# Performance work log

Measured on AMD Instinct MI355X. Metric: run time of the kernel, lower is better.

The kernel has to match this reference:

```python
import jax, jax.numpy as jnp
import numpy as np

N_NODES = 100000
N_EDGES = 300000
F_IN = 128
H = 256
L = 3


def setup_inputs() -> dict:
    key = jax.random.key(0)
    ks = jax.random.split(key, 8)
    s = 0.05
    return {
        "x": jax.random.normal(ks[0], (N_NODES, F_IN), dtype=jnp.float32),
        "edge_index": jax.random.randint(ks[1], (2, N_EDGES), 0, N_NODES, dtype=jnp.int32),
        "enc_w1": jax.random.normal(ks[2], (F_IN, H), dtype=jnp.float32) * s,
        "enc_b1": jnp.zeros((H,), dtype=jnp.float32),
        "enc_w2": jax.random.normal(ks[3], (H, H), dtype=jnp.float32) * s,
        "enc_b2": jnp.zeros((H,), dtype=jnp.float32),
        "gcn_w": jax.random.normal(ks[4], (L, H, H), dtype=jnp.float32) * s,
        "gcn_b": jnp.zeros((L, H), dtype=jnp.float32),
    }


def reference(x, edge_index, enc_w1, enc_b1, enc_w2, enc_b2, gcn_w, gcn_b):
    N = x.shape[0]
    # node_encoder: Linear -> ReLU -> (Dropout=id in eval) -> Linear
    h = jax.nn.relu(x @ enc_w1 + enc_b1) @ enc_w2 + enc_b2  # [N, H]

    # GCNConv normalization with self-loops (PyG default)
    loops = jnp.arange(N, dtype=edge_index.dtype)
    src = jnp.concatenate([edge_index[0], loops])  # [E+N]
    dst = jnp.concatenate([edge_index[1], loops])
    deg = jax.ops.segment_sum(jnp.ones_like(dst, dtype=h.dtype), dst, num_segments=N)
    dinv = jnp.where(deg > 0, jax.lax.rsqrt(deg), 0.0)
    norm = (dinv[src] * dinv[dst])[:, None]  # [E+N, 1]

    num_layers = gcn_w.shape[0]
    for l in range(num_layers):
        m = h @ gcn_w[l]  # transform [N, H]
        # gather messages from src, normalize, scatter-add to dst
        h = jax.ops.segment_sum(m[src] * norm, dst, num_segments=N) + gcn_b[l]
        h = jax.nn.relu(h)  # dropout is identity in eval mode
    return h
```

## Files before the change

### kernel.cpp

```cpp
#include <hip/hip_runtime.h>
#include <hip/hip_bf16.h>

#define NNODES 100000
#define NEDGES 300000
#define FIN 128
#define HDIM 256
#define NLAYERS 3
#define MPAD 100096

typedef float f32x4 __attribute__((ext_vector_type(4)));
typedef short bf16x8 __attribute__((ext_vector_type(8)));

__device__ inline float bf2f(unsigned short u) {
    union { unsigned int i; float f; } v;
    v.i = ((unsigned int)u) << 16;
    return v.f;
}
__device__ inline unsigned short f2bf(float f) {
    union { float f; unsigned int i; } v;
    v.f = f;
    return (unsigned short)((v.i + 0x7fffu + ((v.i >> 16) & 1u)) >> 16);
}

__device__ __forceinline__ void gll16(const unsigned short* g, unsigned short* l) {
    __builtin_amdgcn_global_load_lds(
        (const __attribute__((address_space(1))) unsigned int*)g,
        (__attribute__((address_space(3))) unsigned int*)l, 16, 0, 0);
}

template <int K, bool BIAS, bool RELU>
__global__ __launch_bounds__(256) void gemm_lds_k(
    const unsigned short* __restrict__ A, const unsigned short* __restrict__ Bt,
    const float* __restrict__ bias, unsigned short* __restrict__ C) {
    constexpr int BK = 32;
    constexpr int NT = K / BK;
    __shared__ unsigned short sA[3][128 * BK];
    __shared__ unsigned short sB[3][128 * BK];

    const int tid  = threadIdx.x;
    const int lane = tid & 63;
    const int wid  = tid >> 6;
    const int r15  = lane & 15;
    const int kq   = lane >> 4;
    const int wr   = wid >> 1;
    const int wc   = wid & 1;
    const int rowblk = blockIdx.y * 128;
    const int colblk = blockIdx.x * 128;

    const unsigned short* gA[2];
    const unsigned short* gB[2];
    int ldsbase[2];
#pragma unroll
    for (int q = 0; q < 2; ++q) {
        int rr   = q * 64 + wid * 16 + (lane >> 2);
        int slot = (lane & 3) ^ ((rr >> 1) & 3);
        gA[q] = A  + (size_t)(rowblk + rr) * K + slot * 8;
        gB[q] = Bt + (size_t)(colblk + rr) * K + slot * 8;
        ldsbase[q] = (q * 64 + wid * 16) * BK;
    }

    const int sread = ((kq ^ ((r15 >> 1) & 3)) * 8);
    int aoff[4], boff[4];
#pragma unroll
    for (int i = 0; i < 4; ++i) {
        aoff[i] = (wr * 64 + i * 16 + r15) * BK + sread;
        boff[i] = (wc * 64 + i * 16 + r15) * BK + sread;
    }

    f32x4 acc[4][4] = {};

#pragma unroll
    for (int q = 0; q < 2; ++q) {
        gll16(gA[q], &sA[0][ldsbase[q]]);
        gll16(gB[q], &sB[0][ldsbase[q]]);
    }
#pragma unroll
    for (int q = 0; q < 2; ++q) {
        gll16(gA[q] + BK, &sA[1][ldsbase[q]]);
        gll16(gB[q] + BK, &sB[1][ldsbase[q]]);
    }

#pragma unroll
    for (int t = 0; t < NT; ++t) {
        if (t + 1 < NT) {
            asm volatile("s_waitcnt vmcnt(4)" ::: "memory");
        } else {
            asm volatile("s_waitcnt vmcnt(0)" ::: "memory");
        }
        __builtin_amdgcn_s_barrier();
        if (t + 2 < NT) {
#pragma unroll
            for (int q = 0; q < 2; ++q) {
                gll16(gA[q] + (t + 2) * BK, &sA[(t + 2) % 3][ldsbase[q]]);
                gll16(gB[q] + (t + 2) * BK, &sB[(t + 2) % 3][ldsbase[q]]);
            }
        }
        bf16x8 a[4], b[4];
#pragma unroll
        for (int i = 0; i < 4; ++i) a[i] = *(const bf16x8*)&sA[t % 3][aoff[i]];
#pragma unroll
        for (int j = 0; j < 4; ++j) b[j] = *(const bf16x8*)&sB[t % 3][boff[j]];
#pragma unroll
        for (int i = 0; i < 4; ++i)
#pragma unroll
            for (int j = 0; j < 4; ++j)
                acc[i][j] = __builtin_amdgcn_mfma_f32_16x16x32_bf16(a[i], b[j], acc[i][j], 0, 0, 0);
    }

#pragma unroll
    for (int i = 0; i < 4; ++i) {
#pragma unroll
        for (int reg = 0; reg < 4; ++reg) {
            int row = rowblk + wr * 64 + i * 16 + kq * 4 + reg;
#pragma unroll
            for (int j = 0; j < 4; ++j) {
                int col = colblk + wc * 64 + j * 16 + r15;
                float v = acc[i][j][reg];
                if (BIAS) v += bias[col];
                if (RELU) v = fmaxf(v, 0.0f);
                C[(size_t)row * HDIM + col] = f2bf(v);
            }
        }
    }
}

__global__ void wprep_k(const float* __restrict__ W, unsigned short* __restrict__ Wt,
                        int K, int total) {
    int i = blockIdx.x * blockDim.x + threadIdx.x;
    if (i >= total) return;
    int mat = i / (K * 256);
    int r = i - mat * (K * 256);
    int k = r >> 8, p = r & 255;
    Wt[(size_t)mat * K * 256 + (size_t)p * K + k] = f2bf(W[i]);
}

__global__ void conv_k(const float* __restrict__ W, unsigned short* __restrict__ o, int n4) {
    int i = blockIdx.x * blockDim.x + threadIdx.x;
    if (i >= n4) return;
    float4 v = ((const float4*)W)[i];
    ushort4 u;
    u.x = f2bf(v.x); u.y = f2bf(v.y); u.z = f2bf(v.z); u.w = f2bf(v.w);
    ((ushort4*)o)[i] = u;
}

__global__ void foldbias_k(const float* __restrict__ b2, const float* __restrict__ g0,
                           float* __restrict__ fb) {
    int c = threadIdx.x;
    float s = 0.0f;
#pragma unroll 8
    for (int j = 0; j < HDIM; ++j) s += b2[j] * g0[(size_t)j * HDIM + c];
    fb[c] = s;
}

__global__ void zero_k(unsigned* __restrict__ p, int n) {
    int i = blockIdx.x * blockDim.x + threadIdx.x;
    if (i < n) p[i] = 0u;
}

__global__ void count_k(const int* __restrict__ dst, unsigned* __restrict__ cnt, int E) {
    int e = blockIdx.x * blockDim.x + threadIdx.x;
    if (e < E) atomicAdd(&cnt[dst[e]], 1u);
}

__global__ __launch_bounds__(256) void scan1_k(unsigned* __restrict__ cnt,
                                               int* __restrict__ rs,
                                               unsigned* __restrict__ blocksum,
                                               float* __restrict__ dinv, int N) {
    __shared__ unsigned tmp[256];
    int tid = threadIdx.x;
    int gid = blockIdx.x * 256 + tid;
    unsigned v = (gid < N) ? cnt[gid] : 0u;
    if (gid < N) {
        dinv[gid] = 1.0f / sqrtf((float)(v + 1u));
        cnt[gid] = 0u;
    }
    tmp[tid] = v;
    __syncthreads();
#pragma unroll
    for (int off = 1; off < 256; off <<= 1) {
        unsigned t = (tid >= off) ? tmp[tid - off] : 0u;
        __syncthreads();
        tmp[tid] += t;
        __syncthreads();
    }
    if (gid < N) rs[gid] = (int)(tmp[tid] - v);
    if (tid == 255) blocksum[blockIdx.x] = tmp[tid];
}

__global__ __launch_bounds__(512) void scan2_k(unsigned* __restrict__ blocksum, int nb) {
    __shared__ unsigned tmp[512];
    int tid = threadIdx.x;
    unsigned v = (tid < nb) ? blocksum[tid] : 0u;
    tmp[tid] = v;
    __syncthreads();
#pragma unroll
    for (int off = 1; off < 512; off <<= 1) {
        unsigned t = (tid >= off) ? tmp[tid - off] : 0u;
        __syncthreads();
        tmp[tid] += t;
        __syncthreads();
    }
    if (tid < nb) blocksum[tid] = tmp[tid] - v;
}

__global__ void scan3_k(int* __restrict__ rs, const unsigned* __restrict__ blocksum, int N, int E) {
    int gid = blockIdx.x * blockDim.x + threadIdx.x;
    if (gid < N) rs[gid] += (int)blocksum[gid >> 8];
    if (gid == 0) rs[N] = E;
}

__global__ void fill_k(const int* __restrict__ src, const int* __restrict__ dst,
                       const int* __restrict__ rs, unsigned* __restrict__ cursor,
                       const float* __restrict__ dinv,
                       int2* __restrict__ edata, int E) {
    int e = blockIdx.x * blockDim.x + threadIdx.x;
    if (e >= E) return;
    int s = src[e], d = dst[e];
    int pos = rs[d] + (int)atomicAdd(&cursor[d], 1u);
    float w = dinv[s] * dinv[d];
    edata[pos] = make_int2(s, __float_as_int(w));
}

template <bool OUTF32>
__global__ __launch_bounds__(256) void gather_k(const int* __restrict__ rs,
                                                const int2* __restrict__ edata,
                                                const float* __restrict__ dinv,
                                                const unsigned short* __restrict__ m,
                                                const float* __restrict__ bias,
                                                void* __restrict__ out, int N) {
    int node = blockIdx.x * 4 + (threadIdx.x >> 6);
    int lane = threadIdx.x & 63;
    if (node >= N) return;
    int beg = rs[node], end = rs[node + 1];
    float d = dinv[node];
    float w0 = d * d;
    ushort4 u = ((const ushort4*)(m + (size_t)node * HDIM))[lane];
    float ax = bf2f(u.x) * w0, ay = bf2f(u.y) * w0, az = bf2f(u.z) * w0, aw = bf2f(u.w) * w0;

    for (int base = beg; base < end; base += 64) {
        int2 ed = (base + lane < end) ? edata[base + lane] : make_int2(0, 0);
        int take = end - base;
        if (take > 64) take = 64;
        for (int e = 0; e < take; e += 4) {
            int s0 = __shfl(ed.x, e + 0);
            int s1 = __shfl(ed.x, e + 1);
            int s2 = __shfl(ed.x, e + 2);
            int s3 = __shfl(ed.x, e + 3);
            float wq0 = __int_as_float(__shfl(ed.y, e + 0));
            float wq1 = __int_as_float(__shfl(ed.y, e + 1));
            float wq2 = __int_as_float(__shfl(ed.y, e + 2));
            float wq3 = __int_as_float(__shfl(ed.y, e + 3));
            ushort4 v0 = ((const ushort4*)(m + (size_t)s0 * HDIM))[lane];
            ushort4 v1 = ((const ushort4*)(m + (size_t)s1 * HDIM))[lane];
            ushort4 v2 = ((const ushort4*)(m + (size_t)s2 * HDIM))[lane];
            ushort4 v3 = ((const ushort4*)(m + (size_t)s3 * HDIM))[lane];
            ax += bf2f(v0.x) * wq0; ay += bf2f(v0.y) * wq0;
            az += bf2f(v0.z) * wq0; aw += bf2f(v0.w) * wq0;
            ax += bf2f(v1.x) * wq1; ay += bf2f(v1.y) * wq1;
            az += bf2f(v1.z) * wq1; aw += bf2f(v1.w) * wq1;
            ax += bf2f(v2.x) * wq2; ay += bf2f(v2.y) * wq2;
            az += bf2f(v2.z) * wq2; aw += bf2f(v2.w) * wq2;
            ax += bf2f(v3.x) * wq3; ay += bf2f(v3.y) * wq3;
            az += bf2f(v3.z) * wq3; aw += bf2f(v3.w) * wq3;
        }
    }

    float4 b = ((const float4*)bias)[lane];
    ax = fmaxf(ax + b.x, 0.0f);
    ay = fmaxf(ay + b.y, 0.0f);
    az = fmaxf(az + b.z, 0.0f);
    aw = fmaxf(aw + b.w, 0.0f);
    if (OUTF32) {
        float4 o = {ax, ay, az, aw};
        ((float4*)out)[(size_t)node * 64 + lane] = o;
    } else {
        ushort4 o;
        o.x = f2bf(ax); o.y = f2bf(ay); o.z = f2bf(az); o.w = f2bf(aw);
        ((ushort4*)out)[(size_t)node * 64 + lane] = o;
    }
}

extern "C" void kernel_launch(void* const* d_in, const int* in_sizes, int n_in,
                              void* d_out, int out_size, void* d_ws, size_t ws_size,
                              hipStream_t stream) {
    const float* x  = (const float*)d_in[0];
    const int* ei   = (const int*)d_in[1];
    const float* w1 = (const float*)d_in[2];
    const float* b1 = (const float*)d_in[3];
    const float* w2 = (const float*)d_in[4];
    const float* b2 = (const float*)d_in[5];
    const float* gw = (const float*)d_in[6];
    const float* gb = (const float*)d_in[7];

    const int N = NNODES, E = NEDGES;
    const int* src = ei;
    const int* dst = ei + E;

    char* p = (char*)d_ws;
    unsigned short* h1   = (unsigned short*)p; p += (size_t)MPAD * HDIM * 2;
    unsigned short* h    = (unsigned short*)p; p += (size_t)MPAD * HDIM * 2;
    unsigned short* m    = (unsigned short*)p; p += (size_t)MPAD * HDIM * 2;
    unsigned short* w1t  = (unsigned short*)p; p += (size_t)FIN * HDIM * 2;
    unsigned short* gwt  = (unsigned short*)p; p += (size_t)NLAYERS * HDIM * HDIM * 2;
    unsigned short* w2c  = (unsigned short*)p; p += (size_t)HDIM * HDIM * 2;
    unsigned short* fBt  = (unsigned short*)p; p += (size_t)HDIM * HDIM * 2;
    float* foldb = (float*)p;          p += (size_t)HDIM * 4;
    unsigned* cnt = (unsigned*)p;      p += (size_t)N * 4;
    float* dinv = (float*)p;           p += (size_t)N * 4;
    int* rs = (int*)p;                 p += (size_t)(N + 1) * 4 + 12;
    unsigned* blocksum = (unsigned*)p; p += 512 * 4;
    int2* edata = (int2*)p;            p += (size_t)E * 8;

    unsigned short* xb = m;

    const int nb = (N + 255) / 256;
    const dim3 ggrid(2, MPAD / 128);

    wprep_k<<<(FIN * 256 + 255) / 256, 256, 0, stream>>>(w1, w1t, FIN, FIN * 256);
    wprep_k<<<(NLAYERS * HDIM * 256 + 255) / 256, 256, 0, stream>>>(gw, gwt, HDIM, NLAYERS * HDIM * 256);
    conv_k<<<(HDIM * HDIM / 4 + 255) / 256, 256, 0, stream>>>(w2, w2c, HDIM * HDIM / 4);
    conv_k<<<(N * FIN / 4 + 255) / 256, 256, 0, stream>>>(x, xb, N * FIN / 4);

    foldbias_k<<<1, 256, 0, stream>>>(b2, gw, foldb);
    gemm_lds_k<HDIM, false, false><<<dim3(2, 2), 256, 0, stream>>>(gwt, w2c, nullptr, fBt);

    zero_k<<<nb, 256, 0, stream>>>(cnt, N);
    count_k<<<(E + 255) / 256, 256, 0, stream>>>(dst, cnt, E);
    scan1_k<<<nb, 256, 0, stream>>>(cnt, rs, blocksum, dinv, N);
    scan2_k<<<1, 512, 0, stream>>>(blocksum, nb);
    scan3_k<<<nb + 1, 256, 0, stream>>>(rs, blocksum, N, E);
    fill_k<<<(E + 255) / 256, 256, 0, stream>>>(src, dst, rs, cnt, dinv, edata, E);

    gemm_lds_k<FIN, true, true><<<ggrid, 256, 0, stream>>>(xb, w1t, b1, h1);

    gemm_lds_k<HDIM, true, false><<<ggrid, 256, 0, stream>>>(h1, fBt, foldb, m);
    gather_k<false><<<(N + 3) / 4, 256, 0, stream>>>(rs, edata, dinv, m, gb, h, N);

    for (int l = 1; l < NLAYERS; ++l) {
        const unsigned short* wl = gwt + (size_t)l * HDIM * HDIM;
        const float* bl = gb + (size_t)l * HDIM;
        gemm_lds_k<HDIM, false, false><<<ggrid, 256, 0, stream>>>(h, wl, nullptr, m);
        if (l < NLAYERS - 1)
            gather_k<false><<<(N + 3) / 4, 256, 0, stream>>>(rs, edata, dinv, m, bl, h, N);
        else
            gather_k<true><<<(N + 3) / 4, 256, 0, stream>>>(rs, edata, dinv, m, bl, d_out, N);
    }
}
```

Before: 459.8 us.

## Widen GEMM tile to full 256 columns with 512-thread blocks and vectorized stores

The GEMM kernel now uses 8 waves per block covering a 128x256 output tile, so each block spans the full hidden width and the grid drops to one column block. Each A row tile is loaded once instead of twice across column blocks. The MFMA operands are swapped so each lane holds four consecutive columns, which allows packed 4-element bf16 stores and a float4 bias load. The trade-off is more LDS per block (B tile doubled) and fewer blocks in flight, which may lower occupancy.

```diff
diff --git a/kernel.cpp b/kernel.cpp
--- a/kernel.cpp
+++ b/kernel.cpp
@@ -29,34 +29,36 @@
 }
 
 template <int K, bool BIAS, bool RELU>
-__global__ __launch_bounds__(256) void gemm_lds_k(
+__global__ __launch_bounds__(512, 4) void gemm_lds_k(
     const unsigned short* __restrict__ A, const unsigned short* __restrict__ Bt,
     const float* __restrict__ bias, unsigned short* __restrict__ C) {
     constexpr int BK = 32;
     constexpr int NT = K / BK;
     __shared__ unsigned short sA[3][128 * BK];
-    __shared__ unsigned short sB[3][128 * BK];
+    __shared__ unsigned short sB[3][256 * BK];
 
     const int tid  = threadIdx.x;
     const int lane = tid & 63;
     const int wid  = tid >> 6;
     const int r15  = lane & 15;
     const int kq   = lane >> 4;
-    const int wr   = wid >> 1;
-    const int wc   = wid & 1;
+    const int wr   = wid >> 2;
+    const int wc   = wid & 3;
     const int rowblk = blockIdx.y * 128;
-    const int colblk = blockIdx.x * 128;
-
-    const unsigned short* gA[2];
+
+    int rA = wid * 16 + (lane >> 2);
+    int sltA = (lane & 3) ^ ((rA >> 1) & 3);
+    const unsigned short* gA = A + (size_t)(rowblk + rA) * K + sltA * 8;
+    const int ldsA = wid * 16 * BK;
+
     const unsigned short* gB[2];
-    int ldsbase[2];
+    int ldsB[2];
 #pragma unroll
     for (int q = 0; q < 2; ++q) {
-        int rr   = q * 64 + wid * 16 + (lane >> 2);
-        int slot = (lane & 3) ^ ((rr >> 1) & 3);
-        gA[q] = A  + (size_t)(rowblk + rr) * K + slot * 8;
-        gB[q] = Bt + (size_t)(colblk + rr) * K + slot * 8;
-        ldsbase[q] = (q * 64 + wid * 16) * BK;
+        int rB = wid * 32 + q * 16 + (lane >> 2);
+        int sltB = (lane & 3) ^ ((rB >> 1) & 3);
+        gB[q] = Bt + (size_t)rB * K + sltB * 8;
+        ldsB[q] = (wid * 32 + q * 16) * BK;
     }
 
     const int sread = ((kq ^ ((r15 >> 1) & 3)) * 8);
@@ -70,30 +72,24 @@
     f32x4 acc[4][4] = {};
 
 #pragma unroll
-    for (int q = 0; q < 2; ++q) {
-        gll16(gA[q], &sA[0][ldsbase[q]]);
-        gll16(gB[q], &sB[0][ldsbase[q]]);
-    }
-#pragma unroll
-    for (int q = 0; q < 2; ++q) {
-        gll16(gA[q] + BK, &sA[1][ldsbase[q]]);
-        gll16(gB[q] + BK, &sB[1][ldsbase[q]]);
+    for (int s = 0; s < 2; ++s) {
+        gll16(gA + s * BK, &sA[s][ldsA]);
+        gll16(gB[0] + s * BK, &sB[s][ldsB[0]]);
+        gll16(gB[1] + s * BK, &sB[s][ldsB[1]]);
     }
 
 #pragma unroll
     for (int t = 0; t < NT; ++t) {
         if (t + 1 < NT) {
-            asm volatile("s_waitcnt vmcnt(4)" ::: "memory");
+            asm volatile("s_waitcnt vmcnt(3)" ::: "memory");
         } else {
             asm volatile("s_waitcnt vmcnt(0)" ::: "memory");
         }
         __builtin_amdgcn_s_barrier();
         if (t + 2 < NT) {
-#pragma unroll
-            for (int q = 0; q < 2; ++q) {
-                gll16(gA[q] + (t + 2) * BK, &sA[(t + 2) % 3][ldsbase[q]]);
-                gll16(gB[q] + (t + 2) * BK, &sB[(t + 2) % 3][ldsbase[q]]);
-            }
+            gll16(gA + (t + 2) * BK, &sA[(t + 2) % 3][ldsA]);
+            gll16(gB[0] + (t + 2) * BK, &sB[(t + 2) % 3][ldsB[0]]);
+            gll16(gB[1] + (t + 2) * BK, &sB[(t + 2) % 3][ldsB[1]]);
         }
         bf16x8 a[4], b[4];
 #pragma unroll
@@ -104,22 +100,27 @@
         for (int i = 0; i < 4; ++i)
 #pragma unroll
             for (int j = 0; j < 4; ++j)
-                acc[i][j] = __builtin_amdgcn_mfma_f32_16x16x32_bf16(a[i], b[j], acc[i][j], 0, 0, 0);
+                acc[i][j] = __builtin_amdgcn_mfma_f32_16x16x32_bf16(b[j], a[i], acc[i][j], 0, 0, 0);
     }
 
 #pragma unroll
     for (int i = 0; i < 4; ++i) {
-#pragma unroll
-        for (int reg = 0; reg < 4; ++reg) {
-            int row = rowblk + wr * 64 + i * 16 + kq * 4 + reg;
-#pragma unroll
-            for (int j = 0; j < 4; ++j) {
-                int col = colblk + wc * 64 + j * 16 + r15;
-                float v = acc[i][j][reg];
-                if (BIAS) v += bias[col];
-                if (RELU) v = fmaxf(v, 0.0f);
-                C[(size_t)row * HDIM + col] = f2bf(v);
+        int row = rowblk + wr * 64 + i * 16 + r15;
+#pragma unroll
+        for (int j = 0; j < 4; ++j) {
+            int colb = wc * 64 + j * 16 + kq * 4;
+            float v0 = acc[i][j][0], v1 = acc[i][j][1], v2 = acc[i][j][2], v3 = acc[i][j][3];
+            if (BIAS) {
+                float4 bb = ((const float4*)bias)[colb >> 2];
+                v0 += bb.x; v1 += bb.y; v2 += bb.z; v3 += bb.w;
             }
+            if (RELU) {
+                v0 = fmaxf(v0, 0.0f); v1 = fmaxf(v1, 0.0f);
+                v2 = fmaxf(v2, 0.0f); v3 = fmaxf(v3, 0.0f);
+            }
+            ushort4 o;
+            o.x = f2bf(v0); o.y = f2bf(v1); o.z = f2bf(v2); o.w = f2bf(v3);
+            *(ushort4*)&C[(size_t)row * HDIM + colb] = o;
         }
     }
 }
@@ -314,7 +315,7 @@
     unsigned short* xb = m;
 
     const int nb = (N + 255) / 256;
-    const dim3 ggrid(2, MPAD / 128);
+    const dim3 ggrid(1, MPAD / 128);
 
     wprep_k<<<(FIN * 256 + 255) / 256, 256, 0, stream>>>(w1, w1t, FIN, FIN * 256);
     wprep_k<<<(NLAYERS * HDIM * 256 + 255) / 256, 256, 0, stream>>>(gw, gwt, HDIM, NLAYERS * HDIM * 256);
@@ -322,7 +323,7 @@
     conv_k<<<(N * FIN / 4 + 255) / 256, 256, 0, stream>>>(x, xb, N * FIN / 4);
 
     foldbias_k<<<1, 256, 0, stream>>>(b2, gw, foldb);
-    gemm_lds_k<HDIM, false, false><<<dim3(2, 2), 256, 0, stream>>>(gwt, w2c, nullptr, fBt);
+    gemm_lds_k<HDIM, false, false><<<dim3(1, 2), 512, 0, stream>>>(gwt, w2c, nullptr, fBt);
 
     zero_k<<<nb, 256, 0, stream>>>(cnt, N);
     count_k<<<(E + 255) / 256, 256, 0, stream>>>(dst, cnt, E);
@@ -331,15 +332,15 @@
     scan3_k<<<nb + 1, 256, 0, stream>>>(rs, blocksum, N, E);
     fill_k<<<(E + 255) / 256, 256, 0, stream>>>(src, dst, rs, cnt, dinv, edata, E);
 
-    gemm_lds_k<FIN, true, true><<<ggrid, 256, 0, stream>>>(xb, w1t, b1, h1);
-
-    gemm_lds_k<HDIM, true, false><<<ggrid, 256, 0, stream>>>(h1, fBt, foldb, m);
+    gemm_lds_k<FIN, true, true><<<ggrid, 512, 0, stream>>>(xb, w1t, b1, h1);
+
+    gemm_lds_k<HDIM, true, false><<<ggrid, 512, 0, stream>>>(h1, fBt, foldb, m);
     gather_k<false><<<(N + 3) / 4, 256, 0, stream>>>(rs, edata, dinv, m, gb, h, N);
 
     for (int l = 1; l < NLAYERS; ++l) {
         const unsigned short* wl = gwt + (size_t)l * HDIM * HDIM;
         const float* bl = gb + (size_t)l * HDIM;
-        gemm_lds_k<HDIM, false, false><<<ggrid, 256, 0, stream>>>(h, wl, nullptr, m);
+        gemm_lds_k<HDIM, false, false><<<ggrid, 512, 0, stream>>>(h, wl, nullptr, m);
         if (l < NLAYERS - 1)
             gather_k<false><<<(N + 3) / 4, 256, 0, stream>>>(rs, edata, dinv, m, bl, h, N);
         else
```

After: 484.6 us. 1.05x slower.

## Fuse weight-prep launches and remap GEMM tiles so column pairs run adjacently

Applied to the files above, without the earlier changes.

Merges the weight transposes, w2 conversion, counter zeroing and bias folding into a single prep kernel, removing four small launches. The GEMMs move to a 1D grid with a swizzled block-to-tile mapping, so both column tiles of each group of 8 row tiles are scheduled close together and reuse the same A rows in cache. The mapping pads the grid and needs an early-exit guard. Tiny launches cost little on the critical path, so the effect is likely modest.

```diff
diff --git a/kernel.cpp b/kernel.cpp
--- a/kernel.cpp
+++ b/kernel.cpp
@@ -31,11 +31,18 @@
 template <int K, bool BIAS, bool RELU>
 __global__ __launch_bounds__(256) void gemm_lds_k(
     const unsigned short* __restrict__ A, const unsigned short* __restrict__ Bt,
-    const float* __restrict__ bias, unsigned short* __restrict__ C) {
+    const float* __restrict__ bias, unsigned short* __restrict__ C, int my) {
     constexpr int BK = 32;
     constexpr int NT = K / BK;
     __shared__ unsigned short sA[3][128 * BK];
     __shared__ unsigned short sB[3][128 * BK];
+
+    const int bid   = blockIdx.x;
+    const int ytile = (bid >> 4) * 8 + (bid & 7);
+    if (ytile >= my) return;
+    const int xcol  = (bid >> 3) & 1;
+    const int rowblk = ytile * 128;
+    const int colblk = xcol * 128;
 
     const int tid  = threadIdx.x;
     const int lane = tid & 63;
@@ -44,8 +51,6 @@
     const int kq   = lane >> 4;
     const int wr   = wid >> 1;
     const int wc   = wid & 1;
-    const int rowblk = blockIdx.y * 128;
-    const int colblk = blockIdx.x * 128;
 
     const unsigned short* gA[2];
     const unsigned short* gB[2];
@@ -124,14 +129,40 @@
     }
 }
 
-__global__ void wprep_k(const float* __restrict__ W, unsigned short* __restrict__ Wt,
-                        int K, int total) {
-    int i = blockIdx.x * blockDim.x + threadIdx.x;
-    if (i >= total) return;
-    int mat = i / (K * 256);
-    int r = i - mat * (K * 256);
-    int k = r >> 8, p = r & 255;
-    Wt[(size_t)mat * K * 256 + (size_t)p * K + k] = f2bf(W[i]);
+__global__ __launch_bounds__(256) void prep_k(
+    const float* __restrict__ w1, unsigned short* __restrict__ w1t,
+    const float* __restrict__ gw, unsigned short* __restrict__ gwt,
+    const float* __restrict__ w2, unsigned short* __restrict__ w2c,
+    const float* __restrict__ b2, float* __restrict__ foldb,
+    unsigned* __restrict__ cnt) {
+    int b = blockIdx.x;
+    int tid = threadIdx.x;
+    if (b < 128) {
+        int i = b * 256 + tid;
+        int k = i >> 8, p = i & 255;
+        w1t[(size_t)p * FIN + k] = f2bf(w1[i]);
+    } else if (b < 896) {
+        int i = (b - 128) * 256 + tid;
+        int mat = i >> 16;
+        int r = i & 65535;
+        int k = r >> 8, p = r & 255;
+        gwt[(size_t)mat * 65536 + (size_t)p * HDIM + k] = f2bf(gw[i]);
+    } else if (b < 960) {
+        int i = (b - 896) * 256 + tid;
+        float4 v = ((const float4*)w2)[i];
+        ushort4 u;
+        u.x = f2bf(v.x); u.y = f2bf(v.y); u.z = f2bf(v.z); u.w = f2bf(v.w);
+        ((ushort4*)w2c)[i] = u;
+    } else if (b < 1351) {
+        int i = (b - 960) * 256 + tid;
+        if (i < NNODES) cnt[i] = 0u;
+    } else {
+        int c = tid;
+        float s = 0.0f;
+#pragma unroll 8
+        for (int j = 0; j < HDIM; ++j) s += b2[j] * gw[(size_t)j * HDIM + c];
+        foldb[c] = s;
+    }
 }
 
 __global__ void conv_k(const float* __restrict__ W, unsigned short* __restrict__ o, int n4) {
@@ -141,20 +172,6 @@
     ushort4 u;
     u.x = f2bf(v.x); u.y = f2bf(v.y); u.z = f2bf(v.z); u.w = f2bf(v.w);
     ((ushort4*)o)[i] = u;
-}
-
-__global__ void foldbias_k(const float* __restrict__ b2, const float* __restrict__ g0,
-                           float* __restrict__ fb) {
-    int c = threadIdx.x;
-    float s = 0.0f;
-#pragma unroll 8
-    for (int j = 0; j < HDIM; ++j) s += b2[j] * g0[(size_t)j * HDIM + c];
-    fb[c] = s;
-}
-
-__global__ void zero_k(unsigned* __restrict__ p, int n) {
-    int i = blockIdx.x * blockDim.x + threadIdx.x;
-    if (i < n) p[i] = 0u;
 }
 
 __global__ void count_k(const int* __restrict__ dst, unsigned* __restrict__ cnt, int E) {
@@ -314,32 +331,29 @@
     unsigned short* xb = m;
 
     const int nb = (N + 255) / 256;
-    const dim3 ggrid(2, MPAD / 128);
-
-    wprep_k<<<(FIN * 256 + 255) / 256, 256, 0, stream>>>(w1, w1t, FIN, FIN * 256);
-    wprep_k<<<(NLAYERS * HDIM * 256 + 255) / 256, 256, 0, stream>>>(gw, gwt, HDIM, NLAYERS * HDIM * 256);
-    conv_k<<<(HDIM * HDIM / 4 + 255) / 256, 256, 0, stream>>>(w2, w2c, HDIM * HDIM / 4);
+    const int MY = MPAD / 128;
+    const int ggrid = 16 * ((MY + 7) / 8);
+
+    prep_k<<<1352, 256, 0, stream>>>(w1, w1t, gw, gwt, w2, w2c, b2, foldb, cnt);
     conv_k<<<(N * FIN / 4 + 255) / 256, 256, 0, stream>>>(x, xb, N * FIN / 4);
 
-    foldbias_k<<<1, 256, 0, stream>>>(b2, gw, foldb);
-    gemm_lds_k<HDIM, false, false><<<dim3(2, 2), 256, 0, stream>>>(gwt, w2c, nullptr, fBt);
-
-    zero_k<<<nb, 256, 0, stream>>>(cnt, N);
+    gemm_lds_k<HDIM, false, false><<<16, 256, 0, stream>>>(gwt, w2c, nullptr, fBt, 2);
+
     count_k<<<(E + 255) / 256, 256, 0, stream>>>(dst, cnt, E);
     scan1_k<<<nb, 256, 0, stream>>>(cnt, rs, blocksum, dinv, N);
     scan2_k<<<1, 512, 0, stream>>>(blocksum, nb);
     scan3_k<<<nb + 1, 256, 0, stream>>>(rs, blocksum, N, E);
     fill_k<<<(E + 255) / 256, 256, 0, stream>>>(src, dst, rs, cnt, dinv, edata, E);
 
-    gemm_lds_k<FIN, true, true><<<ggrid, 256, 0, stream>>>(xb, w1t, b1, h1);
-
-    gemm_lds_k<HDIM, true, false><<<ggrid, 256, 0, stream>>>(h1, fBt, foldb, m);
+    gemm_lds_k<FIN, true, true><<<ggrid, 256, 0, stream>>>(xb, w1t, b1, h1, MY);
+
+    gemm_lds_k<HDIM, true, false><<<ggrid, 256, 0, stream>>>(h1, fBt, foldb, m, MY);
     gather_k<false><<<(N + 3) / 4, 256, 0, stream>>>(rs, edata, dinv, m, gb, h, N);
 
     for (int l = 1; l < NLAYERS; ++l) {
         const unsigned short* wl = gwt + (size_t)l * HDIM * HDIM;
         const float* bl = gb + (size_t)l * HDIM;
-        gemm_lds_k<HDIM, false, false><<<ggrid, 256, 0, stream>>>(h, wl, nullptr, m);
+        gemm_lds_k<HDIM, false, false><<<ggrid, 256, 0, stream>>>(h, wl, nullptr, m, MY);
         if (l < NLAYERS - 1)
             gather_k<false><<<(N + 3) / 4, 256, 0, stream>>>(rs, edata, dinv, m, bl, h, N);
         else
```

Measured after the change: 436.3 us. -5.1%, faster.
